# Optimization experiments

Hardware: AMD Instinct MI355X
Metric: run time of the kernel (lower is better)

The kernel has to match this reference:

```python
import jax, jax.numpy as jnp
import numpy as np

NU = 100000
NV = 100000
D = 128
R = 5          # num_support (rating levels)
O = 64         # output_dim // num_support
E = 640000     # edges per relation


def setup_inputs() -> dict:
    key = jax.random.key(0)
    ks = jax.random.split(key, 7)
    x_u = jax.random.normal(ks[0], (NU, D), dtype=jnp.float32)
    x_v = jax.random.normal(ks[1], (NV, D), dtype=jnp.float32)
    sup_rows = jax.random.randint(ks[2], (R, E), 0, NU, dtype=jnp.int32)
    sup_cols = jax.random.randint(ks[3], (R, E), 0, NV, dtype=jnp.int32)
    sup_vals = jax.random.uniform(ks[4], (R, E), dtype=jnp.float32)
    weights_u = jax.random.normal(ks[5], (R, D, O), dtype=jnp.float32)
    weights_v = jax.random.normal(ks[6], (R, D, O), dtype=jnp.float32)
    return {"x_u": x_u, "x_v": x_v, "sup_rows": sup_rows, "sup_cols": sup_cols,
            "sup_vals": sup_vals, "weights_u": weights_u, "weights_v": weights_v}


def _spmm(rows, cols, vals, feat, num_segments):
    # sparse [num_segments, n_src] @ feat [n_src, O] via gather + segment_sum
    return jax.ops.segment_sum(vals[:, None] * feat[cols], rows,
                               num_segments=num_segments)


def reference(x_u, x_v, sup_rows, sup_cols, sup_vals, weights_u, weights_v):
    # ordinal weight accumulation: wu_i = sum_{j<=i} weights_u[j]
    Wu = jnp.cumsum(weights_u, axis=0)  # [R, D, O]
    Wv = jnp.cumsum(weights_v, axis=0)  # [R, D, O]
    tmp_u = jnp.einsum('nd,rdo->rno', x_u, Wu)  # [R, NU, O]
    tmp_v = jnp.einsum('md,rdo->rmo', x_v, Wv)  # [R, NV, O]
    # z_u = sum_r support[r] @ tmp_v[r];  z_v = sum_r support[r]^T @ tmp_u[r]
    z_u = jax.vmap(lambda r, c, v, f: _spmm(r, c, v, f, NU))(
        sup_rows, sup_cols, sup_vals, tmp_v).sum(axis=0)
    z_v = jax.vmap(lambda r, c, v, f: _spmm(r, c, v, f, NV))(
        sup_cols, sup_rows, sup_vals, tmp_u).sum(axis=0)
    return jax.nn.relu(z_u), jax.nn.relu(z_v)
```

## Files before the change

### kernel.cpp

```cpp
#include <hip/hip_runtime.h>
#include <hip/hip_bf16.h>

#define R_SUP 5
#define D_IN 128
#define O_OUT 64
#define NBMAX 512
#define CHUNK 8192

typedef __attribute__((ext_vector_type(8))) short bf16x8;
typedef __attribute__((ext_vector_type(4))) float f32x4;

__device__ __forceinline__ unsigned short f2bf(float f) {
  union { float f; unsigned int u; } c; c.f = f;
  unsigned int u = c.u;
  return (unsigned short)((u + 0x7FFFu + ((u >> 16) & 1u)) >> 16);
}
__device__ __forceinline__ float bf2f(unsigned short h) {
  return __uint_as_float(((unsigned int)h) << 16);
}

__global__ __launch_bounds__(256) void cumsum_w(
    const float* __restrict__ wu, const float* __restrict__ wv,
    float* __restrict__ wcu, float* __restrict__ wcv,
    unsigned short* __restrict__ wtbu, unsigned short* __restrict__ wtbv) {
  int i = blockIdx.x * 256 + threadIdx.x;
  if (i >= D_IN * O_OUT) return;
  const int d = i >> 6;
  const int o = i & 63;
  float su = 0.f, sv = 0.f;
#pragma unroll
  for (int r = 0; r < R_SUP; ++r) {
    su += wu[r * D_IN * O_OUT + i];
    sv += wv[r * D_IN * O_OUT + i];
    wcu[r * D_IN * O_OUT + i] = su;
    wcv[r * D_IN * O_OUT + i] = sv;
    wtbu[((size_t)r * O_OUT + o) * D_IN + d] = f2bf(su);
    wtbv[((size_t)r * O_OUT + o) * D_IN + d] = f2bf(sv);
  }
}

__global__ __launch_bounds__(256) void cvt_bf16(
    const float* __restrict__ x, unsigned short* __restrict__ y, int n4) {
  int i = blockIdx.x * 256 + threadIdx.x;
  int stride = gridDim.x * 256;
  for (; i < n4; i += stride) {
    float4 v = ((const float4*)x)[i];
    ushort4 h;
    h.x = f2bf(v.x); h.y = f2bf(v.y); h.z = f2bf(v.z); h.w = f2bf(v.w);
    ((ushort4*)y)[i] = h;
  }
}

__global__ __launch_bounds__(256) void zero_f32(float* __restrict__ p, int n4) {
  int i = blockIdx.x * 256 + threadIdx.x;
  int stride = gridDim.x * 256;
  float4 z = make_float4(0.f, 0.f, 0.f, 0.f);
  for (; i < n4; i += stride) ((float4*)p)[i] = z;
}

__global__ __launch_bounds__(256) void zero_i32(int* __restrict__ p, int n) {
  int i = blockIdx.x * 256 + threadIdx.x;
  int stride = gridDim.x * 256;
  for (; i < n; i += stride) p[i] = 0;
}

__global__ __launch_bounds__(256) void gemm5_mfma(
    const unsigned short* __restrict__ xbf,
    const unsigned short* __restrict__ wtb,
    unsigned short* __restrict__ tmp5, size_t strideR, int N) {
  const int row0 = blockIdx.x * 64;
  const int wave = threadIdx.x >> 6;
  const int lane = threadIdx.x & 63;
  const int m = lane & 15;
  const int q = lane >> 4;
  const int o0 = wave * 16;

  bf16x8 a[4][4];
#pragma unroll
  for (int rt = 0; rt < 4; ++rt) {
    int row = row0 + rt * 16 + m;
    if (row >= N) row = N - 1;
    const unsigned short* px = xbf + (size_t)row * D_IN + q * 8;
#pragma unroll
    for (int k0 = 0; k0 < 4; ++k0)
      a[rt][k0] = *(const bf16x8*)(px + k0 * 32);
  }

  for (int r = 0; r < R_SUP; ++r) {
    bf16x8 b[4];
    const unsigned short* pw =
        wtb + ((size_t)r * O_OUT + o0 + m) * D_IN + q * 8;
#pragma unroll
    for (int k0 = 0; k0 < 4; ++k0)
      b[k0] = *(const bf16x8*)(pw + k0 * 32);
    unsigned short* pz = tmp5 + (size_t)r * strideR;
#pragma unroll
    for (int rt = 0; rt < 4; ++rt) {
      f32x4 acc = {0.f, 0.f, 0.f, 0.f};
#pragma unroll
      for (int k0 = 0; k0 < 4; ++k0)
        acc = __builtin_amdgcn_mfma_f32_16x16x32_bf16(a[rt][k0], b[k0], acc,
                                                      0, 0, 0);
#pragma unroll
      for (int reg = 0; reg < 4; ++reg) {
        int row = row0 + rt * 16 + q * 4 + reg;
        if (row < N) pz[(size_t)row * O_OUT + o0 + m] = f2bf(acc[reg]);
      }
    }
  }
}

__global__ __launch_bounds__(256) void coarse_hist(
    const int* __restrict__ rows, const int* __restrict__ cols,
    int* __restrict__ cnt_u, int* __restrict__ cnt_v, int nE5,
    int nbu, int nbv) {
  __shared__ int hu[NBMAX], hv[NBMAX];
  const int tid = threadIdx.x;
  for (int t = tid; t < NBMAX; t += 256) { hu[t] = 0; hv[t] = 0; }
  __syncthreads();
  const int n4 = nE5 >> 2;
  int i = blockIdx.x * 256 + tid;
  int stride = gridDim.x * 256;
  for (; i < n4; i += stride) {
    int4 rr = ((const int4*)rows)[i];
    int4 cc = ((const int4*)cols)[i];
    atomicAdd(&hu[rr.x >> 8], 1); atomicAdd(&hu[rr.y >> 8], 1);
    atomicAdd(&hu[rr.z >> 8], 1); atomicAdd(&hu[rr.w >> 8], 1);
    atomicAdd(&hv[cc.x >> 8], 1); atomicAdd(&hv[cc.y >> 8], 1);
    atomicAdd(&hv[cc.z >> 8], 1); atomicAdd(&hv[cc.w >> 8], 1);
  }
  for (i = (n4 << 2) + blockIdx.x * 256 + tid; i < nE5; i += stride) {
    atomicAdd(&hu[rows[i] >> 8], 1);
    atomicAdd(&hv[cols[i] >> 8], 1);
  }
  __syncthreads();
  for (int t = tid; t < nbu; t += 256) if (hu[t]) atomicAdd(&cnt_u[t], hu[t]);
  for (int t = tid; t < nbv; t += 256) if (hv[t]) atomicAdd(&cnt_v[t], hv[t]);
}

__global__ __launch_bounds__(512) void coarse_scan(
    int* __restrict__ cnt_u, int* __restrict__ cnt_v,
    int* __restrict__ cb_u, int* __restrict__ cb_v,
    int* __restrict__ gcur_u, int* __restrict__ gcur_v, int nbu, int nbv) {
  int* cnt = blockIdx.x ? cnt_v : cnt_u;
  int* cb  = blockIdx.x ? cb_v  : cb_u;
  int* gc  = blockIdx.x ? gcur_v : gcur_u;
  int nb   = blockIdx.x ? nbv   : nbu;
  __shared__ int sc[NBMAX];
  const int t = threadIdx.x;
  sc[t] = (t < nb) ? cnt[t] : 0;
  __syncthreads();
  for (int off = 1; off < NBMAX; off <<= 1) {
    int add = (t >= off) ? sc[t - off] : 0;
    __syncthreads();
    sc[t] += add;
    __syncthreads();
  }
  int excl = t ? sc[t - 1] : 0;
  if (t < nb) { cb[t] = excl; gc[t] = excl; }
  if (t == 0) cb[nb] = sc[NBMAX - 1];
}

__global__ __launch_bounds__(512) void coarse_scatter(
    const int* __restrict__ rows, const int* __restrict__ cols,
    const float* __restrict__ vals, int* __restrict__ gcur_u,
    int* __restrict__ gcur_v, int2* __restrict__ mid_u,
    int2* __restrict__ mid_v, int nE5, int E, int nbu, int nbv) {
  __shared__ int2 buf[CHUNK];
  __shared__ int h[NBMAX], sc[NBMAX], gb[NBMAX], cur[NBMAX];
  const int tid = threadIdx.x;
  const int dir = blockIdx.x & 1;
  const int base = (blockIdx.x >> 1) * CHUNK;
  const int end = min(base + CHUNK, nE5);
  const int E2 = 2 * E, E3 = 3 * E, E4 = 4 * E;

  const int* ids   = dir ? cols : rows;
  const int* other = dir ? rows : cols;
  int* gcur = dir ? gcur_v : gcur_u;
  int2* mid = dir ? mid_v : mid_u;
  const int nb = dir ? nbv : nbu;

  h[tid] = 0;
  __syncthreads();
  for (int i = base + tid; i < end; i += 512)
    atomicAdd(&h[ids[i] >> 8], 1);
  __syncthreads();
  sc[tid] = h[tid];
  __syncthreads();
  for (int off = 1; off < NBMAX; off <<= 1) {
    int add = (tid >= off) ? sc[tid - off] : 0;
    __syncthreads();
    sc[tid] += add;
    __syncthreads();
  }
  int excl = tid ? sc[tid - 1] : 0;
  cur[tid] = excl;
  if (tid < nb && h[tid]) gb[tid] = atomicAdd(&gcur[tid], h[tid]);
  __syncthreads();
  for (int i = base + tid; i < end; i += 512) {
    int id = ids[i];
    int src = other[i];
    int vb = __float_as_int(vals[i]);
    int r = (i >= E) + (i >= E2) + (i >= E3) + (i >= E4);
    int pos = atomicAdd(&cur[id >> 8], 1);
    buf[pos] = make_int2(((id & 255) << 20) | (r << 17) | src, vb);
  }
  __syncthreads();
  const int wv = tid >> 6;
  const int lane = tid & 63;
  for (int b = wv; b < nb; b += 8) {
    int s = b ? sc[b - 1] : 0;
    int e = sc[b];
    if (s == e) continue;
    int2* dst = mid + gb[b];
    for (int j = s + lane; j < e; j += 64) dst[j - s] = buf[j];
  }
}

__global__ __launch_bounds__(256) void fine_scatter(
    const int2* __restrict__ mid, const int* __restrict__ cb,
    int* __restrict__ rp, int2* __restrict__ fin, int nbuck, int Ndst,
    int strideR) {
  __shared__ int h[256], sc[256], cur[256];
  const int tid = threadIdx.x;
  const int b = blockIdx.x;
  const int s = cb[b];
  const int e2 = cb[b + 1];
  h[tid] = 0;
  __syncthreads();
  for (int i = s + tid; i < e2; i += 256)
    atomicAdd(&h[(mid[i].x >> 20) & 255], 1);
  __syncthreads();
  sc[tid] = h[tid];
  __syncthreads();
  for (int off = 1; off < 256; off <<= 1) {
    int add = (tid >= off) ? sc[tid - off] : 0;
    __syncthreads();
    sc[tid] += add;
    __syncthreads();
  }
  int excl = tid ? sc[tid - 1] : 0;
  int d = b * 256 + tid;
  if (d <= Ndst) rp[d] = s + excl;
  if (b == nbuck - 1 && tid == 0 && Ndst >= nbuck * 256) rp[Ndst] = cb[nbuck];
  cur[tid] = s + excl;
  __syncthreads();
  for (int i = s + tid; i < e2; i += 256) {
    int2 pk = mid[i];
    int dl = (pk.x >> 20) & 255;
    int r = (pk.x >> 17) & 7;
    int src = pk.x & 0x1FFFF;
    int pos = atomicAdd(&cur[dl], 1);
    fin[pos] = make_int2(r * strideR + (src << 6), pk.y);
  }
}

__global__ __launch_bounds__(256) void spmm_pull_bf16(
    const int* __restrict__ rp, const int2* __restrict__ ep,
    const unsigned short* __restrict__ tmp5,
    float* __restrict__ z, int Ndst) {
  int g = (blockIdx.x * 256 + threadIdx.x) >> 4;
  int lane = threadIdx.x & 15;
  if (g >= Ndst) return;
  int s = rp[g];
  int e = rp[g + 1];
  const unsigned short* tl = tmp5 + lane * 4;
  float4 acc = make_float4(0.f, 0.f, 0.f, 0.f);
  int i = s;
  for (; i + 8 <= e; i += 8) {
    int2 pk[8];
#pragma unroll
    for (int j = 0; j < 8; ++j) pk[j] = ep[i + j];
    ushort4 h[8];
#pragma unroll
    for (int j = 0; j < 8; ++j)
      h[j] = *(const ushort4*)(tl + (unsigned)pk[j].x);
#pragma unroll
    for (int j = 0; j < 8; ++j) {
      float v = __int_as_float(pk[j].y);
      acc.x += v * bf2f(h[j].x);
      acc.y += v * bf2f(h[j].y);
      acc.z += v * bf2f(h[j].z);
      acc.w += v * bf2f(h[j].w);
    }
  }
  for (; i < e; ++i) {
    int2 pk = ep[i];
    float v = __int_as_float(pk.y);
    ushort4 h = *(const ushort4*)(tl + (unsigned)pk.x);
    acc.x += v * bf2f(h.x);
    acc.y += v * bf2f(h.y);
    acc.z += v * bf2f(h.z);
    acc.w += v * bf2f(h.w);
  }
  acc.x = acc.x > 0.f ? acc.x : 0.f;
  acc.y = acc.y > 0.f ? acc.y : 0.f;
  acc.z = acc.z > 0.f ? acc.z : 0.f;
  acc.w = acc.w > 0.f ? acc.w : 0.f;
  ((float4*)(z + (size_t)g * O_OUT))[lane] = acc;
}

__global__ __launch_bounds__(256) void gemm64(
    const float* __restrict__ x, const float* __restrict__ w,
    float* __restrict__ out, int N) {
  __shared__ float sXT[D_IN][68];
  __shared__ float sW[D_IN][O_OUT];
  const int tid = threadIdx.x;
  const int row0 = blockIdx.x * 64;
  for (int i = tid; i < 2048; i += 256) {
    int d = i >> 4;
    int o4 = i & 15;
    ((float4*)&sW[d][0])[o4] = ((const float4*)w)[i];
  }
  for (int i = tid; i < 2048; i += 256) {
    int rl = i >> 5;
    int d4 = i & 31;
    int row = row0 + rl;
    float4 xv = make_float4(0.f, 0.f, 0.f, 0.f);
    if (row < N) xv = ((const float4*)x)[(size_t)row * 32 + d4];
    sXT[d4 * 4 + 0][rl] = xv.x;
    sXT[d4 * 4 + 1][rl] = xv.y;
    sXT[d4 * 4 + 2][rl] = xv.z;
    sXT[d4 * 4 + 3][rl] = xv.w;
  }
  __syncthreads();
  const int col4 = (tid & 15) * 4;
  const int row4 = (tid >> 4) * 4;
  float acc[4][4] = {};
#pragma unroll 8
  for (int d = 0; d < D_IN; ++d) {
    float4 xv = *(const float4*)&sXT[d][row4];
    float4 wv = *(const float4*)&sW[d][col4];
    acc[0][0] += xv.x * wv.x; acc[0][1] += xv.x * wv.y; acc[0][2] += xv.x * wv.z; acc[0][3] += xv.x * wv.w;
    acc[1][0] += xv.y * wv.x; acc[1][1] += xv.y * wv.y; acc[1][2] += xv.y * wv.z; acc[1][3] += xv.y * wv.w;
    acc[2][0] += xv.z * wv.x; acc[2][1] += xv.z * wv.y; acc[2][2] += xv.z * wv.z; acc[2][3] += xv.z * wv.w;
    acc[3][0] += xv.w * wv.x; acc[3][1] += xv.w * wv.y; acc[3][2] += xv.w * wv.z; acc[3][3] += xv.w * wv.w;
  }
#pragma unroll
  for (int i = 0; i < 4; ++i) {
    int row = row0 + row4 + i;
    if (row < N)
      *(float4*)&out[row * O_OUT + col4] =
          make_float4(acc[i][0], acc[i][1], acc[i][2], acc[i][3]);
  }
}

__global__ __launch_bounds__(256) void spmm_push(
    const int* __restrict__ dst, const int* __restrict__ src,
    const float* __restrict__ vals, const float* __restrict__ tmp,
    float* __restrict__ z, int E) {
  int t = blockIdx.x * 256 + threadIdx.x;
  int e = t >> 4;
  int lane = t & 15;
  if (e >= E) return;
  int d_ = dst[e];
  int s_ = src[e];
  float v = vals[e];
  float4 f = ((const float4*)tmp)[s_ * 16 + lane];
  float* zp = z + (size_t)d_ * O_OUT + lane * 4;
  atomicAdd(zp + 0, v * f.x);
  atomicAdd(zp + 1, v * f.y);
  atomicAdd(zp + 2, v * f.z);
  atomicAdd(zp + 3, v * f.w);
}

__global__ __launch_bounds__(256) void relu_f32(float* __restrict__ p, int n4) {
  int i = blockIdx.x * 256 + threadIdx.x;
  int stride = gridDim.x * 256;
  for (; i < n4; i += stride) {
    float4 v = ((float4*)p)[i];
    v.x = v.x > 0.f ? v.x : 0.f;
    v.y = v.y > 0.f ? v.y : 0.f;
    v.z = v.z > 0.f ? v.z : 0.f;
    v.w = v.w > 0.f ? v.w : 0.f;
    ((float4*)p)[i] = v;
  }
}

extern "C" void kernel_launch(void* const* d_in, const int* in_sizes, int n_in,
                              void* d_out, int out_size, void* d_ws, size_t ws_size,
                              hipStream_t stream) {
  const float* x_u      = (const float*)d_in[0];
  const float* x_v      = (const float*)d_in[1];
  const int*   sup_rows = (const int*)d_in[2];
  const int*   sup_cols = (const int*)d_in[3];
  const float* sup_vals = (const float*)d_in[4];
  const float* wu       = (const float*)d_in[5];
  const float* wv       = (const float*)d_in[6];

  const int NU = in_sizes[0] / D_IN;
  const int NV = in_sizes[1] / D_IN;
  const int E  = in_sizes[2] / R_SUP;
  const int Nmax = NU > NV ? NU : NV;
  const int nE5 = R_SUP * E;
  const int nbu = (NU + 255) / 256;
  const int nbv = (NV + 255) / 256;
  const int nbmax = nbu > nbv ? nbu : nbv;

  float* out = (float*)d_out;
  float* z_u = out;
  float* z_v = out + (size_t)NU * O_OUT;

  const int WDO = R_SUP * D_IN * O_OUT;
  const size_t strideR = (size_t)Nmax * O_OUT;
  const size_t bpad = (size_t)nbmax + 16;

  const size_t midu_bytes_raw = (size_t)nE5 * 8;
  const size_t xbf_bytes = (size_t)Nmax * D_IN * 2;
  const size_t midu_bytes = ((midu_bytes_raw > xbf_bytes ? midu_bytes_raw
                                                         : xbf_bytes) + 255) & ~(size_t)255;

  const size_t needR = midu_bytes + (size_t)nE5 * 16 + strideR * R_SUP * 2 +
                       (size_t)2 * WDO * 4 + (size_t)2 * WDO * 2 +
                       ((size_t)Nmax + 16) * 4 + 6 * bpad * 4 + 512;

  if (ws_size >= needR && nbmax <= NBMAX && Nmax < (1 << 17)) {
    char* base = (char*)d_ws;
    int2* mid_u = (int2*)base;
    unsigned short* xbf = (unsigned short*)base;
    int2* mid_v = (int2*)(base + midu_bytes);
    int2* fin   = mid_v + nE5;
    unsigned short* tmp5 = (unsigned short*)(fin + nE5);
    float* wcu = (float*)(tmp5 + strideR * R_SUP);
    float* wcv = wcu + WDO;
    unsigned short* wtbu = (unsigned short*)(wcv + WDO);
    unsigned short* wtbv = wtbu + WDO;
    int* rp    = (int*)(wtbv + WDO);
    int* cnt_u = rp + Nmax + 16;
    int* cnt_v = cnt_u + bpad;
    int* cb_u  = cnt_v + bpad;
    int* cb_v  = cb_u + bpad;
    int* gcur_u = cb_v + bpad;
    int* gcur_v = gcur_u + bpad;

    cumsum_w<<<(D_IN * O_OUT + 255) / 256, 256, 0, stream>>>(
        wu, wv, wcu, wcv, wtbu, wtbv);
    zero_i32<<<(2 * (int)bpad + 255) / 256, 256, 0, stream>>>(cnt_u, 2 * (int)bpad);
    coarse_hist<<<512, 256, 0, stream>>>(sup_rows, sup_cols, cnt_u, cnt_v,
                                         nE5, nbu, nbv);
    coarse_scan<<<2, 512, 0, stream>>>(cnt_u, cnt_v, cb_u, cb_v, gcur_u,
                                       gcur_v, nbu, nbv);
    coarse_scatter<<<2 * ((nE5 + CHUNK - 1) / CHUNK), 512, 0, stream>>>(
        sup_rows, sup_cols, sup_vals, gcur_u, gcur_v, mid_u, mid_v, nE5, E,
        nbu, nbv);

    fine_scatter<<<nbu, 256, 0, stream>>>(mid_u, cb_u, rp, fin, nbu, NU,
                                          (int)strideR);
    cvt_bf16<<<1024, 256, 0, stream>>>(x_v, xbf, NV * D_IN / 4);
    gemm5_mfma<<<(NV + 63) / 64, 256, 0, stream>>>(xbf, wtbv, tmp5, strideR, NV);
    spmm_pull_bf16<<<(NU * 16 + 255) / 256, 256, 0, stream>>>(
        rp, fin, tmp5, z_u, NU);

    fine_scatter<<<nbv, 256, 0, stream>>>(mid_v, cb_v, rp, fin, nbv, NV,
                                          (int)strideR);
    cvt_bf16<<<1024, 256, 0, stream>>>(x_u, xbf, NU * D_IN / 4);
    gemm5_mfma<<<(NU + 63) / 64, 256, 0, stream>>>(xbf, wtbu, tmp5, strideR, NU);
    spmm_pull_bf16<<<(NV * 16 + 255) / 256, 256, 0, stream>>>(
        rp, fin, tmp5, z_v, NV);
  } else {
    float* wcu = (float*)d_ws;
    float* wcv = wcu + WDO;
    unsigned short* wtbu = (unsigned short*)(wcv + WDO);
    unsigned short* wtbv = wtbu + WDO;
    float* tmp = (float*)(wtbv + WDO);
    const int n4_out = out_size / 4;
    cumsum_w<<<(D_IN * O_OUT + 255) / 256, 256, 0, stream>>>(
        wu, wv, wcu, wcv, wtbu, wtbv);
    zero_f32<<<1024, 256, 0, stream>>>(out, n4_out);
    const int spmm_blocks = (E * 16 + 255) / 256;
    for (int r = 0; r < R_SUP; ++r) {
      const int* rws = sup_rows + (size_t)r * E;
      const int* cls = sup_cols + (size_t)r * E;
      const float* vls = sup_vals + (size_t)r * E;
      gemm64<<<(NV + 63) / 64, 256, 0, stream>>>(x_v, wcv + r * D_IN * O_OUT, tmp, NV);
      spmm_push<<<spmm_blocks, 256, 0, stream>>>(rws, cls, vls, tmp, z_u, E);
      gemm64<<<(NU + 63) / 64, 256, 0, stream>>>(x_u, wcu + r * D_IN * O_OUT, tmp, NU);
      spmm_push<<<spmm_blocks, 256, 0, stream>>>(cls, rws, vls, tmp, z_v, E);
    }
    relu_f32<<<1024, 256, 0, stream>>>(out, n4_out);
  }
}
```

Baseline: 545.7 us.

## Fuse bf16 conversion into MFMA GEMM, stage stores in LDS, widen SpMM gathers

Removes the separate fp32-to-bf16 conversion kernel by having the MFMA GEMM load fp32 inputs and convert them in registers, which drops one full read and write of the input features per side. GEMM outputs are staged in shared memory and written as 16-byte coalesced stores instead of scattered 2-byte stores, at the cost of two block barriers per rating level. The pull SpMM now uses 8 lanes per destination with 16-byte gathers instead of 16 lanes with 8-byte gathers. That halves the thread count and the per-edge index loads, but each lane does more work.

New measurement: 556.2 us. Within noise of the previous version (+1.9%).

```diff
diff --git a/kernel.cpp b/kernel.cpp
--- a/kernel.cpp
+++ b/kernel.cpp
@@ -8,6 +8,7 @@
 #define CHUNK 8192
 
 typedef __attribute__((ext_vector_type(8))) short bf16x8;
+typedef __attribute__((ext_vector_type(8))) unsigned short u16x8;
 typedef __attribute__((ext_vector_type(4))) float f32x4;
 
 __device__ __forceinline__ unsigned short f2bf(float f) {
@@ -39,18 +40,6 @@
   }
 }
 
-__global__ __launch_bounds__(256) void cvt_bf16(
-    const float* __restrict__ x, unsigned short* __restrict__ y, int n4) {
-  int i = blockIdx.x * 256 + threadIdx.x;
-  int stride = gridDim.x * 256;
-  for (; i < n4; i += stride) {
-    float4 v = ((const float4*)x)[i];
-    ushort4 h;
-    h.x = f2bf(v.x); h.y = f2bf(v.y); h.z = f2bf(v.z); h.w = f2bf(v.w);
-    ((ushort4*)y)[i] = h;
-  }
-}
-
 __global__ __launch_bounds__(256) void zero_f32(float* __restrict__ p, int n4) {
   int i = blockIdx.x * 256 + threadIdx.x;
   int stride = gridDim.x * 256;
@@ -65,12 +54,14 @@
 }
 
 __global__ __launch_bounds__(256) void gemm5_mfma(
-    const unsigned short* __restrict__ xbf,
+    const float* __restrict__ x,
     const unsigned short* __restrict__ wtb,
     unsigned short* __restrict__ tmp5, size_t strideR, int N) {
+  __shared__ unsigned short st[64][72];
+  const int tid = threadIdx.x;
   const int row0 = blockIdx.x * 64;
-  const int wave = threadIdx.x >> 6;
-  const int lane = threadIdx.x & 63;
+  const int wave = tid >> 6;
+  const int lane = tid & 63;
   const int m = lane & 15;
   const int q = lane >> 4;
   const int o0 = wave * 16;
@@ -80,11 +71,22 @@
   for (int rt = 0; rt < 4; ++rt) {
     int row = row0 + rt * 16 + m;
     if (row >= N) row = N - 1;
-    const unsigned short* px = xbf + (size_t)row * D_IN + q * 8;
-#pragma unroll
-    for (int k0 = 0; k0 < 4; ++k0)
-      a[rt][k0] = *(const bf16x8*)(px + k0 * 32);
-  }
+    const float* px = x + (size_t)row * D_IN + q * 8;
+#pragma unroll
+    for (int k0 = 0; k0 < 4; ++k0) {
+      float4 f0 = *(const float4*)(px + k0 * 32);
+      float4 f1 = *(const float4*)(px + k0 * 32 + 4);
+      bf16x8 t;
+      t[0] = (short)f2bf(f0.x); t[1] = (short)f2bf(f0.y);
+      t[2] = (short)f2bf(f0.z); t[3] = (short)f2bf(f0.w);
+      t[4] = (short)f2bf(f1.x); t[5] = (short)f2bf(f1.y);
+      t[6] = (short)f2bf(f1.z); t[7] = (short)f2bf(f1.w);
+      a[rt][k0] = t;
+    }
+  }
+
+  const int rr = tid >> 2;
+  const int c0 = (tid & 3) * 16;
 
   for (int r = 0; r < R_SUP; ++r) {
     bf16x8 b[4];
@@ -93,7 +95,6 @@
 #pragma unroll
     for (int k0 = 0; k0 < 4; ++k0)
       b[k0] = *(const bf16x8*)(pw + k0 * 32);
-    unsigned short* pz = tmp5 + (size_t)r * strideR;
 #pragma unroll
     for (int rt = 0; rt < 4; ++rt) {
       f32x4 acc = {0.f, 0.f, 0.f, 0.f};
@@ -102,11 +103,16 @@
         acc = __builtin_amdgcn_mfma_f32_16x16x32_bf16(a[rt][k0], b[k0], acc,
                                                       0, 0, 0);
 #pragma unroll
-      for (int reg = 0; reg < 4; ++reg) {
-        int row = row0 + rt * 16 + q * 4 + reg;
-        if (row < N) pz[(size_t)row * O_OUT + o0 + m] = f2bf(acc[reg]);
-      }
+      for (int reg = 0; reg < 4; ++reg)
+        st[rt * 16 + q * 4 + reg][o0 + m] = f2bf(acc[reg]);
     }
+    __syncthreads();
+    if (row0 + rr < N) {
+      unsigned short* pz = tmp5 + (size_t)r * strideR + (size_t)row0 * O_OUT;
+      *(int4*)(pz + rr * O_OUT + c0) = *(const int4*)&st[rr][c0];
+      *(int4*)(pz + rr * O_OUT + c0 + 8) = *(const int4*)&st[rr][c0 + 8];
+    }
+    __syncthreads();
   }
 }
 
@@ -259,45 +265,44 @@
     const int* __restrict__ rp, const int2* __restrict__ ep,
     const unsigned short* __restrict__ tmp5,
     float* __restrict__ z, int Ndst) {
-  int g = (blockIdx.x * 256 + threadIdx.x) >> 4;
-  int lane = threadIdx.x & 15;
+  int g = (blockIdx.x * 256 + threadIdx.x) >> 3;
+  int lane = threadIdx.x & 7;
   if (g >= Ndst) return;
   int s = rp[g];
   int e = rp[g + 1];
-  const unsigned short* tl = tmp5 + lane * 4;
-  float4 acc = make_float4(0.f, 0.f, 0.f, 0.f);
+  const unsigned short* tl = tmp5 + lane * 8;
+  float acc[8] = {0.f, 0.f, 0.f, 0.f, 0.f, 0.f, 0.f, 0.f};
   int i = s;
   for (; i + 8 <= e; i += 8) {
     int2 pk[8];
 #pragma unroll
     for (int j = 0; j < 8; ++j) pk[j] = ep[i + j];
-    ushort4 h[8];
+    u16x8 h[8];
 #pragma unroll
     for (int j = 0; j < 8; ++j)
-      h[j] = *(const ushort4*)(tl + (unsigned)pk[j].x);
+      h[j] = *(const u16x8*)(tl + (unsigned)pk[j].x);
 #pragma unroll
     for (int j = 0; j < 8; ++j) {
       float v = __int_as_float(pk[j].y);
-      acc.x += v * bf2f(h[j].x);
-      acc.y += v * bf2f(h[j].y);
-      acc.z += v * bf2f(h[j].z);
-      acc.w += v * bf2f(h[j].w);
+#pragma unroll
+      for (int k = 0; k < 8; ++k) acc[k] += v * bf2f(h[j][k]);
     }
   }
   for (; i < e; ++i) {
     int2 pk = ep[i];
     float v = __int_as_float(pk.y);
-    ushort4 h = *(const ushort4*)(tl + (unsigned)pk.x);
-    acc.x += v * bf2f(h.x);
-    acc.y += v * bf2f(h.y);
-    acc.z += v * bf2f(h.z);
-    acc.w += v * bf2f(h.w);
-  }
-  acc.x = acc.x > 0.f ? acc.x : 0.f;
-  acc.y = acc.y > 0.f ? acc.y : 0.f;
-  acc.z = acc.z > 0.f ? acc.z : 0.f;
-  acc.w = acc.w > 0.f ? acc.w : 0.f;
-  ((float4*)(z + (size_t)g * O_OUT))[lane] = acc;
+    u16x8 h = *(const u16x8*)(tl + (unsigned)pk.x);
+#pragma unroll
+    for (int k = 0; k < 8; ++k) acc[k] += v * bf2f(h[k]);
+  }
+  float* zp = z + (size_t)g * O_OUT + lane * 8;
+  float4 o0, o1;
+  o0.x = fmaxf(acc[0], 0.f); o0.y = fmaxf(acc[1], 0.f);
+  o0.z = fmaxf(acc[2], 0.f); o0.w = fmaxf(acc[3], 0.f);
+  o1.x = fmaxf(acc[4], 0.f); o1.y = fmaxf(acc[5], 0.f);
+  o1.z = fmaxf(acc[6], 0.f); o1.w = fmaxf(acc[7], 0.f);
+  *(float4*)(zp) = o0;
+  *(float4*)(zp + 4) = o1;
 }
 
 __global__ __launch_bounds__(256) void gemm64(
@@ -405,20 +410,16 @@
   const size_t strideR = (size_t)Nmax * O_OUT;
   const size_t bpad = (size_t)nbmax + 16;
 
-  const size_t midu_bytes_raw = (size_t)nE5 * 8;
-  const size_t xbf_bytes = (size_t)Nmax * D_IN * 2;
-  const size_t midu_bytes = ((midu_bytes_raw > xbf_bytes ? midu_bytes_raw
-                                                         : xbf_bytes) + 255) & ~(size_t)255;
-
-  const size_t needR = midu_bytes + (size_t)nE5 * 16 + strideR * R_SUP * 2 +
+  const size_t mid_bytes = (((size_t)nE5 * 8) + 255) & ~(size_t)255;
+
+  const size_t needR = mid_bytes + (size_t)nE5 * 16 + strideR * R_SUP * 2 +
                        (size_t)2 * WDO * 4 + (size_t)2 * WDO * 2 +
                        ((size_t)Nmax + 16) * 4 + 6 * bpad * 4 + 512;
 
   if (ws_size >= needR && nbmax <= NBMAX && Nmax < (1 << 17)) {
     char* base = (char*)d_ws;
     int2* mid_u = (int2*)base;
-    unsigned short* xbf = (unsigned short*)base;
-    int2* mid_v = (int2*)(base + midu_bytes);
+    int2* mid_v = (int2*)(base + mid_bytes);
     int2* fin   = mid_v + nE5;
     unsigned short* tmp5 = (unsigned short*)(fin + nE5);
     float* wcu = (float*)(tmp5 + strideR * R_SUP);
@@ -446,16 +447,14 @@
 
     fine_scatter<<<nbu, 256, 0, stream>>>(mid_u, cb_u, rp, fin, nbu, NU,
                                           (int)strideR);
-    cvt_bf16<<<1024, 256, 0, stream>>>(x_v, xbf, NV * D_IN / 4);
-    gemm5_mfma<<<(NV + 63) / 64, 256, 0, stream>>>(xbf, wtbv, tmp5, strideR, NV);
-    spmm_pull_bf16<<<(NU * 16 + 255) / 256, 256, 0, stream>>>(
+    gemm5_mfma<<<(NV + 63) / 64, 256, 0, stream>>>(x_v, wtbv, tmp5, strideR, NV);
+    spmm_pull_bf16<<<(NU * 8 + 255) / 256, 256, 0, stream>>>(
         rp, fin, tmp5, z_u, NU);
 
     fine_scatter<<<nbv, 256, 0, stream>>>(mid_v, cb_v, rp, fin, nbv, NV,
                                           (int)strideR);
-    cvt_bf16<<<1024, 256, 0, stream>>>(x_u, xbf, NU * D_IN / 4);
-    gemm5_mfma<<<(NU + 63) / 64, 256, 0, stream>>>(xbf, wtbu, tmp5, strideR, NU);
-    spmm_pull_bf16<<<(NV * 16 + 255) / 256, 256, 0, stream>>>(
+    gemm5_mfma<<<(NU + 63) / 64, 256, 0, stream>>>(x_u, wtbu, tmp5, strideR, NU);
+    spmm_pull_bf16<<<(NV * 8 + 255) / 256, 256, 0, stream>>>(
         rp, fin, tmp5, z_v, NV);
   } else {
     float* wcu = (float*)d_ws;
```
